# Kernel tuning notes

Hardware: AMD Instinct MI355X
Metric: run time of the kernel (lower is better)

The kernel has to match this reference:

```python
import jax, jax.numpy as jnp
import numpy as np

C = 128         # sphere_channels
H = 512         # hidden_channels
EC = 128        # edge_channels
LMAX = 4
K = 4           # num_experts
N_EQ = 2        # ceil(K/2) equivariant experts
N_NE = 2
N_NODES = 8192
N_EDGES = 262144
DEG_SIZES = np.array([2 * l + 1 for l in range(LMAX + 1)])  # [1,3,5,7,9]
M = int(DEG_SIZES.sum())  # 25 coeffs


def setup_inputs() -> dict:
    key = jax.random.key(0)
    ks = jax.random.split(key, 20)
    s = 0.02
    return {
        "x_emb": jax.random.normal(ks[0], (N_NODES, M, C), jnp.float32),
        "t_ij": jax.random.normal(ks[1], (N_EDGES, EC), jnp.float32),
        "edge_index": jax.random.randint(ks[2], (2, N_EDGES), 0, N_NODES, jnp.int32),
        # equivariant experts (stacked on leading expert axis)
        "eq_w1": jax.random.normal(ks[3], (N_EQ, C, H), jnp.float32) * s,
        "eq_gate_w": jax.random.normal(ks[4], (N_EQ, EC, H * (LMAX + 1)), jnp.float32) * s,
        "eq_gate_b": jax.random.normal(ks[5], (N_EQ, H * (LMAX + 1)), jnp.float32) * s,
        "eq_w2": jax.random.normal(ks[6], (N_EQ, H, C), jnp.float32) * s,
        # non-equivariant experts
        "ne_w1": jax.random.normal(ks[7], (N_NE, C, H), jnp.float32) * s,
        "ne_b1": jax.random.normal(ks[8], (N_NE, H), jnp.float32) * s,
        "ne_gate_w": jax.random.normal(ks[9], (N_NE, EC, H), jnp.float32) * s,
        "ne_gate_b": jax.random.normal(ks[10], (N_NE, H), jnp.float32) * s,
        "ne_w2": jax.random.normal(ks[11], (N_NE, H, C), jnp.float32) * s,
        "ne_b2": jax.random.normal(ks[12], (N_NE, C), jnp.float32) * s,
        # router
        "r_w1": jax.random.normal(ks[13], (EC, EC), jnp.float32) * s,
        "r_b1": jax.random.normal(ks[14], (EC,), jnp.float32) * s,
        "r_w2": jax.random.normal(ks[15], (EC, K), jnp.float32) * s,
        "r_b2": jax.random.normal(ks[16], (K,), jnp.float32) * s,
    }


def reference(x_emb, t_ij, edge_index, eq_w1, eq_gate_w, eq_gate_b, eq_w2,
              ne_w1, ne_b1, ne_gate_w, ne_gate_b, ne_w2, ne_b2,
              r_w1, r_b1, r_w2, r_b2):
    N = x_emb.shape[0]
    silu = jax.nn.silu

    # c_i = scatter-mean of t_ij onto destination nodes
    dst = edge_index[1]
    sums = jax.ops.segment_sum(t_ij, dst, num_segments=N)
    cnt = jax.ops.segment_sum(jnp.ones((t_ij.shape[0],), t_ij.dtype), dst, num_segments=N)
    c = sums / jnp.maximum(cnt, 1.0)[:, None]  # [N, EC]

    # soft routing weights from context
    w = jax.nn.softmax(silu(c @ r_w1 + r_b1) @ r_w2 + r_b2, axis=-1)  # [N, K]

    repeats = jnp.asarray(DEG_SIZES)
    is_scalar = (jnp.arange(M) == 0)[:, None]  # l=0 coeff mask, [M,1]

    # --- equivariant experts (vectorized over expert axis e) ---
    h = jnp.einsum('nmc,ech->enmh', x_emb, eq_w1)                      # [e,N,M,H]
    g = silu(jnp.einsum('nc,ecg->eng', c, eq_gate_w) + eq_gate_b[:, None, :])
    g = g.reshape(N_EQ, N, LMAX + 1, H)
    g = jnp.repeat(g, repeats, axis=2, total_repeat_length=M)          # [e,N,M,H]
    h = jnp.where(is_scalar, silu(h), h) * g                           # SiLU only on l=0
    out_eq = jnp.einsum('enmh,ehc->enmc', h, eq_w2)

    # --- non-equivariant experts ---
    h2 = silu(jnp.einsum('nmc,ech->enmh', x_emb, ne_w1) + ne_b1[:, None, None, :])
    g2 = silu(jnp.einsum('nc,ech->enh', c, ne_gate_w) + ne_gate_b[:, None, :])
    h2 = h2 * g2[:, :, None, :]
    out_ne = jnp.einsum('enmh,ehc->enmc', h2, ne_w2) + ne_b2[:, None, None, :]

    # softmax-weighted mixture (equiv experts first, matching ModuleList order)
    out = (jnp.einsum('nk,knmc->nmc', w[:, :N_EQ], out_eq)
           + jnp.einsum('nk,knmc->nmc', w[:, N_EQ:], out_ne))
    return out
```

## Files before the change

### kernel.cpp

```cpp
#include <hip/hip_runtime.h>

#define NNODES 8192
#define NEDGES 262144
#define CCH    128
#define HCH    512
#define GCOLS  6144
#define ROWS   204800
#define XSPAD  136

typedef __bf16 bf16_t;
typedef __bf16 bf16x8 __attribute__((ext_vector_type(8)));
typedef __bf16 bf16x4 __attribute__((ext_vector_type(4)));
typedef float  f32x4  __attribute__((ext_vector_type(4)));

__device__ __forceinline__ float siluf(float x) {
  return x * __builtin_amdgcn_rcpf(1.f + __expf(-x));
}

#define GLOAD_LDS(g, l) __builtin_amdgcn_global_load_lds( \
    (const __attribute__((address_space(1))) void*)(g), \
    (__attribute__((address_space(3))) void*)(l), 16, 0, 0)

constexpr size_t OFF_CSUM  = 0;
constexpr size_t OFF_DEG   = 4194304;
constexpr size_t OFF_OFFS  = 4227072;
constexpr size_t OFF_CUR   = 4263936;
constexpr size_t OFF_EIDS  = 4296704;
constexpr size_t OFF_WRT   = 5345280;
constexpr size_t OFF_CBF   = 5476352;
constexpr size_t OFF_WPT   = 7573504;
constexpr size_t OFF_BPK   = 9146368;
constexpr size_t OFF_W1T   = 9170944;
constexpr size_t OFF_W2T   = 9695232;
constexpr size_t OFF_GATES = 10219520;

__global__ __launch_bounds__(256) void edge_count_kernel(
    const int* __restrict__ edge_index, int* __restrict__ deg)
{
  int e = blockIdx.x * 256 + threadIdx.x;
  int dst = __builtin_nontemporal_load(&edge_index[NEDGES + e]);
  atomicAdd(&deg[dst], 1);
}

__global__ __launch_bounds__(256) void scan_kernel(
    const int* __restrict__ deg, int* __restrict__ offs, int* __restrict__ cur)
{
  __shared__ int part[256];
  int t = threadIdx.x;
  int s = 0;
  #pragma unroll 4
  for (int i = 0; i < 32; ++i) s += deg[t * 32 + i];
  part[t] = s;
  __syncthreads();
  int incl = s;
  for (int off = 1; off < 256; off <<= 1) {
    int u = (t >= off) ? part[t - off] : 0;
    __syncthreads();
    incl += u;
    part[t] = incl;
    __syncthreads();
  }
  int run = incl - s;
  for (int i = 0; i < 32; ++i) {
    int d = deg[t * 32 + i];
    offs[t * 32 + i] = run;
    cur[t * 32 + i]  = run;
    run += d;
  }
  if (t == 255) offs[8192] = run;
}

__global__ __launch_bounds__(256) void edge_fill_kernel(
    const int* __restrict__ edge_index, int* __restrict__ cur, int* __restrict__ eids)
{
  int e = blockIdx.x * 256 + threadIdx.x;
  int dst = __builtin_nontemporal_load(&edge_index[NEDGES + e]);
  int pos = atomicAdd(&cur[dst], 1);
  eids[pos] = e;
}

__global__ __launch_bounds__(256) void gather_mean_kernel(
    const float* __restrict__ t_ij, const int* __restrict__ offs,
    const int* __restrict__ eids, float* __restrict__ csum, bf16_t* __restrict__ cbf)
{
  __shared__ float red[8][128];
  int n = blockIdx.x, tid = threadIdx.x;
  int sub = tid & 31, rp = tid >> 5;
  int o0 = offs[n], o1 = offs[n + 1];
  f32x4 acc = {0.f, 0.f, 0.f, 0.f};
  for (int j = o0 + rp; j < o1; j += 8) {
    int e = __builtin_nontemporal_load(&eids[j]);
    f32x4 v = __builtin_nontemporal_load((const f32x4*)&t_ij[(size_t)e * CCH + sub * 4]);
    #pragma unroll
    for (int q = 0; q < 4; ++q) acc[q] += v[q];
  }
  *(f32x4*)&red[rp][sub * 4] = acc;
  __syncthreads();
  if (rp == 0) {
    float inv = 1.f / fmaxf((float)(o1 - o0), 1.f);
    f32x4 s = {0.f, 0.f, 0.f, 0.f};
    #pragma unroll
    for (int k = 0; k < 8; ++k) {
      f32x4 r = *(const f32x4*)&red[k][sub * 4];
      #pragma unroll
      for (int q = 0; q < 4; ++q) s[q] += r[q];
    }
    f32x4 m;
    bf16x4 mb;
    #pragma unroll
    for (int q = 0; q < 4; ++q) { m[q] = s[q] * inv; mb[q] = (bf16_t)m[q]; }
    *(f32x4*)&csum[(size_t)n * CCH + sub * 4] = m;
    *(bf16x4*)&cbf[(size_t)n * CCH + sub * 4] = mb;
  }
}

__global__ __launch_bounds__(256) void pack_kernel(
    const float* __restrict__ eq_gate_w, const float* __restrict__ ne_gate_w,
    const float* __restrict__ eq_gate_b, const float* __restrict__ ne_gate_b,
    const float* __restrict__ eq_w1, const float* __restrict__ ne_w1,
    const float* __restrict__ eq_w2, const float* __restrict__ ne_w2,
    bf16_t* __restrict__ WpackT, float* __restrict__ bpack,
    bf16_t* __restrict__ w1T, bf16_t* __restrict__ w2c)
{
  __shared__ float tb[32][33];
  int b = blockIdx.x;
  int tid = threadIdx.x, tx = tid & 31, ty = tid >> 5;
  if (b == 1280) {
    #pragma unroll
    for (int it = 0; it < 24; ++it) {
      int j = it * 256 + tid;
      bpack[j] = (j < 5120) ? eq_gate_b[j] : ne_gate_b[j - 5120];
    }
    return;
  }
  const float* src; bf16_t* dst; int stride; bool w2mode = false;
  int c0, h0; size_t dbase;
  if (b < 640) {
    int e = b / 320, r = b % 320, ct = r / 80, ht = r % 80;
    src = eq_gate_w + (size_t)e * 327680; stride = 2560;
    c0 = ct * 32; h0 = ht * 32;
    dbase = ((size_t)e * 2560 + h0) * 128 + c0; dst = WpackT;
  } else if (b < 768) {
    int bb = b - 640, e = bb / 64, r = bb % 64, ct = r / 16, ht = r % 16;
    src = ne_gate_w + (size_t)e * 65536; stride = 512;
    c0 = ct * 32; h0 = ht * 32;
    dbase = ((size_t)(5120 + e * 512) + h0) * 128 + c0; dst = WpackT;
  } else if (b < 1024) {
    int bb = b - 768, e = bb / 64, r = bb % 64, ct = r / 16, ht = r % 16;
    src = (e < 2) ? eq_w1 + (size_t)e * 65536 : ne_w1 + (size_t)(e - 2) * 65536;
    stride = 512;
    c0 = ct * 32; h0 = ht * 32;
    dbase = ((size_t)(e * 512) + h0) * 128 + c0; dst = w1T;
  } else {
    int bb = b - 1024, e = bb / 64, r = bb % 64, ht = r / 4, ct = r % 4;
    src = (e < 2) ? eq_w2 + (size_t)e * 65536 : ne_w2 + (size_t)(e - 2) * 65536;
    stride = 128; w2mode = true;
    c0 = ct * 32; h0 = ht * 32;
    dbase = (size_t)e * 65536 + (size_t)(ht >> 1) * 8192 + (size_t)c0 * 64 + (size_t)(ht & 1) * 32;
    dst = w2c;
  }
  if (!w2mode) {
    #pragma unroll
    for (int p = 0; p < 4; ++p)
      tb[p * 8 + ty][tx] = src[(size_t)(c0 + p * 8 + ty) * stride + h0 + tx];
    __syncthreads();
    #pragma unroll
    for (int p = 0; p < 4; ++p)
      dst[dbase + (size_t)(p * 8 + ty) * 128 + tx] = (bf16_t)tb[tx][p * 8 + ty];
  } else {
    #pragma unroll
    for (int p = 0; p < 4; ++p)
      tb[p * 8 + ty][tx] = src[(size_t)(h0 + p * 8 + ty) * 128 + c0 + tx];
    __syncthreads();
    #pragma unroll
    for (int p = 0; p < 4; ++p)
      dst[dbase + (size_t)(p * 8 + ty) * 64 + tx] = (bf16_t)tb[tx][p * 8 + ty];
  }
}

__global__ __launch_bounds__(128) void router_kernel(
    const float* __restrict__ c,
    const float* __restrict__ r_w1, const float* __restrict__ r_b1,
    const float* __restrict__ r_w2, const float* __restrict__ r_b2,
    float* __restrict__ wroute)
{
  __shared__ float cl[128];
  __shared__ float h1[128];
  __shared__ float lg[4];
  int n = blockIdx.x, tid = threadIdx.x;
  cl[tid] = c[(size_t)n * 128 + tid];
  __syncthreads();
  float a = 0.f;
  #pragma unroll 8
  for (int k = 0; k < 128; ++k) a += cl[k] * r_w1[k * 128 + tid];
  a += r_b1[tid];
  h1[tid] = siluf(a);
  __syncthreads();
  if (tid < 4) {
    float s = 0.f;
    for (int j = 0; j < 128; ++j) s += h1[j] * r_w2[j * 4 + tid];
    lg[tid] = s + r_b2[tid];
  }
  __syncthreads();
  if (tid == 0) {
    float m = fmaxf(fmaxf(lg[0], lg[1]), fmaxf(lg[2], lg[3]));
    float e0 = __expf(lg[0] - m), e1 = __expf(lg[1] - m);
    float e2 = __expf(lg[2] - m), e3 = __expf(lg[3] - m);
    float s = 1.f / (e0 + e1 + e2 + e3);
    f32x4 w = {e0 * s, e1 * s, e2 * s, e3 * s};
    *(f32x4*)&wroute[n * 4] = w;
  }
}

__global__ __launch_bounds__(256, 2) void gate_gemm_kernel(
    const bf16_t* __restrict__ WpackT, const bf16_t* __restrict__ cbf,
    const float* __restrict__ bpack, const float* __restrict__ wroute,
    bf16_t* __restrict__ gates, int n0)
{
  __shared__ bf16_t gt[128 * XSPAD];
  int jt = blockIdx.x, nt = blockIdx.y;
  int tid = threadIdx.x;
  int wave = tid >> 6, lane = tid & 63;
  int wr = wave >> 1, wc = wave & 1;
  int l15 = lane & 15, quad = lane >> 4;
  int ej = (jt < 20) ? 0 : (jt < 40) ? 1 : (jt < 44) ? 2 : 3;

  f32x4 acc[4][4];
  #pragma unroll
  for (int i = 0; i < 4; ++i)
    #pragma unroll
    for (int j = 0; j < 4; ++j) acc[i][j] = {0.f, 0.f, 0.f, 0.f};

  const bf16_t* abase = WpackT + ((size_t)jt * 128 + wr * 64 + l15) * 128 + quad * 8;
  const bf16_t* bbase = cbf + ((size_t)(n0 + nt * 128) + wc * 64 + l15) * 128 + quad * 8;
  float wsc[4];
  #pragma unroll
  for (int tc = 0; tc < 4; ++tc)
    wsc[tc] = wroute[(size_t)(n0 + nt * 128 + wc * 64 + tc * 16 + l15) * 4 + ej];
  #pragma unroll
  for (int ks = 0; ks < 4; ++ks) {
    bf16x8 af[4], bfr[4];
    #pragma unroll
    for (int tr = 0; tr < 4; ++tr) af[tr] = *(const bf16x8*)(abase + (size_t)tr * 16 * 128 + ks * 32);
    #pragma unroll
    for (int tc = 0; tc < 4; ++tc) bfr[tc] = *(const bf16x8*)(bbase + (size_t)tc * 16 * 128 + ks * 32);
    #pragma unroll
    for (int tr = 0; tr < 4; ++tr)
      #pragma unroll
      for (int tc = 0; tc < 4; ++tc)
        acc[tr][tc] = __builtin_amdgcn_mfma_f32_16x16x32_bf16(af[tr], bfr[tc], acc[tr][tc], 0, 0, 0);
  }
  #pragma unroll
  for (int tr = 0; tr < 4; ++tr) {
    int j0 = wr * 64 + tr * 16 + quad * 4;
    int p0 = wr * 64 + quad * 16 + tr * 4;
    f32x4 bb = *(const f32x4*)&bpack[jt * 128 + j0];
    #pragma unroll
    for (int tc = 0; tc < 4; ++tc) {
      int nl = wc * 64 + tc * 16 + l15;
      f32x4 v = acc[tr][tc];
      bf16x4 gv;
      #pragma unroll
      for (int q = 0; q < 4; ++q) gv[q] = (bf16_t)(siluf(v[q] + bb[q]) * wsc[tc]);
      *(bf16x4*)&gt[nl * XSPAD + p0] = gv;
    }
  }
  __syncthreads();
  #pragma unroll
  for (int it = 0; it < 8; ++it) {
    int idx = it * 2048 + tid * 8;
    int lr = idx >> 7, col = idx & 127;
    *(bf16x8*)&gates[((size_t)nt * 128 + lr) * GCOLS + jt * 128 + col] =
        *(const bf16x8*)&gt[lr * XSPAD + col];
  }
}

__global__ __launch_bounds__(512, 2) void fused_experts_kernel(
    const float* __restrict__ x,
    const bf16_t* __restrict__ w1T,
    const bf16_t* __restrict__ w2c,
    const bf16_t* __restrict__ gates,
    const float* __restrict__ wroute,
    const float* __restrict__ ne_b1,
    const float* __restrict__ ne_b2,
    float* __restrict__ out,
    int n0)
{
  __shared__ __align__(16) bf16_t ws1[8192];
  __shared__ __align__(16) bf16_t ws2[8192];
  __shared__ __align__(16) bf16_t hg[8 * 32 * 64];

  const int tid = threadIdx.x;
  const int wave = tid >> 6, lane = tid & 63;
  const int l15 = lane & 15, quad = lane >> 4;
  const int r0 = n0 * 25 + blockIdx.x * 256;
  const int rbase = wave * 32;
  char* hgw = (char*)(hg + wave * 32 * 64);

  int soff1[2], soff2[2];
  #pragma unroll
  for (int i = 0; i < 2; ++i) {
    int p = wave * 2048 + i * 1024 + lane * 16;
    int row1 = p >> 8;
    soff1[i] = (row1 * 256 + ((p & 255) ^ ((row1 & 7) << 4))) >> 1;
    int row2 = p >> 7;
    soff2[i] = (row2 * 128 + ((p & 127) ^ ((row2 & 7) << 4))) >> 1;
  }
  const int swz = (l15 & 7) << 4;
  int colswz[4];
  #pragma unroll
  for (int ks = 0; ks < 4; ++ks) colswz[ks] = (ks * 64 + quad * 16) ^ swz;

  int nloc[2], lidx[2];
  f32x4 rw[2];
  bf16x8 xf[2][4];
  #pragma unroll
  for (int tc = 0; tc < 2; ++tc) {
    int r = r0 + rbase + tc * 16 + l15;
    int n = r / 25;
    int m = r - n * 25;
    nloc[tc] = n - n0;
    lidx[tc] = (m == 0) ? 0 : (m < 4) ? 1 : (m < 9) ? 2 : (m < 16) ? 3 : 4;
    rw[tc] = *(const f32x4*)&wroute[n * 4];
    const float* xr = x + (size_t)r * CCH + quad * 8;
    #pragma unroll
    for (int ks = 0; ks < 4; ++ks) {
      f32x4 a = __builtin_nontemporal_load((const f32x4*)(xr + ks * 32));
      f32x4 b = __builtin_nontemporal_load((const f32x4*)(xr + ks * 32 + 4));
      bf16x8 v;
      #pragma unroll
      for (int q = 0; q < 4; ++q) { v[q] = (bf16_t)a[q]; v[4 + q] = (bf16_t)b[q]; }
      xf[tc][ks] = v;
    }
  }

  auto gaddr = [&](int tc, int tt) -> const bf16_t* {
    int ee = tt >> 3, hh = tt & 7;
    int base = (ee < 2) ? ee * 2560 + lidx[tc] * 512 : 5120 + (ee - 2) * 512;
    return gates + (nloc[tc] * GCOLS + base + hh * 64 + quad * 16);
  };

  f32x4 oacc[8][2];
  #pragma unroll
  for (int i = 0; i < 8; ++i)
    #pragma unroll
    for (int j = 0; j < 2; ++j) oacc[i][j] = {0.f, 0.f, 0.f, 0.f};

  bf16x8 gnxa[2], gnxb[2];
  #pragma unroll
  for (int tc = 0; tc < 2; ++tc) {
    const bf16_t* gp = gaddr(tc, 0);
    gnxa[tc] = *(const bf16x8*)gp;
    gnxb[tc] = *(const bf16x8*)(gp + 8);
  }
  #pragma unroll
  for (int i = 0; i < 2; ++i) {
    GLOAD_LDS(w1T + soff1[i], ws1 + wave * 1024 + i * 512);
    GLOAD_LDS(w2c + soff2[i], ws2 + wave * 1024 + i * 512);
  }
  __syncthreads();

  #pragma unroll 1
  for (int t = 0; t < 32; ++t) {
    const int e = t >> 3, hc = t & 7;
    const bool is_eq = (e < 2);

    bf16x8 ga[2], gb[2];
    #pragma unroll
    for (int tc = 0; tc < 2; ++tc) { ga[tc] = gnxa[tc]; gb[tc] = gnxb[tc]; }
    if (t < 31) {
      #pragma unroll
      for (int tc = 0; tc < 2; ++tc) {
        const bf16_t* gp = gaddr(tc, t + 1);
        gnxa[tc] = *(const bf16x8*)gp;
        gnxb[tc] = *(const bf16x8*)(gp + 8);
      }
    }

    f32x4 hacc[4][2];
    #pragma unroll
    for (int i = 0; i < 4; ++i)
      #pragma unroll
      for (int j = 0; j < 2; ++j) hacc[i][j] = {0.f, 0.f, 0.f, 0.f};
    #pragma unroll
    for (int ks = 0; ks < 4; ++ks) {
      bf16x8 af[4];
      #pragma unroll
      for (int tr = 0; tr < 4; ++tr)
        af[tr] = *(const bf16x8*)((const char*)ws1 + (l15 + tr * 16) * 256 + colswz[ks]);
      #pragma unroll
      for (int tr = 0; tr < 4; ++tr)
        #pragma unroll
        for (int tc = 0; tc < 2; ++tc)
          hacc[tr][tc] = __builtin_amdgcn_mfma_f32_16x16x32_bf16(af[tr], xf[tc][ks], hacc[tr][tc], 0, 0, 0);
    }
    #pragma unroll
    for (int tc = 0; tc < 2; ++tc) {
      #pragma unroll
      for (int tr = 0; tr < 4; ++tr) {
        int hl = tr * 16 + quad * 4;
        f32x4 v = hacc[tr][tc];
        if (is_eq) {
          if (lidx[tc] == 0) {
            #pragma unroll
            for (int q = 0; q < 4; ++q) v[q] = siluf(v[q]);
          }
        } else {
          f32x4 b1 = *(const f32x4*)&ne_b1[(e - 2) * 512 + hc * 64 + hl];
          #pragma unroll
          for (int q = 0; q < 4; ++q) v[q] = siluf(v[q] + b1[q]);
        }
        bf16x4 hv;
        #pragma unroll
        for (int q = 0; q < 4; ++q) {
          float gf = (float)((tr < 2 ? ga[tc] : gb[tc])[(tr & 1) * 4 + q]);
          hv[q] = (bf16_t)(v[q] * gf);
        }
        *(bf16x4*)(hgw + (tc * 16 + l15) * 128 + ((tr * 32 + quad * 8) ^ swz)) = hv;
      }
    }
    __syncthreads();
    if (t < 31) {
      const bf16_t* g1 = w1T + ((size_t)(t + 1) << 13);
      #pragma unroll
      for (int i = 0; i < 2; ++i)
        GLOAD_LDS(g1 + soff1[i], ws1 + wave * 1024 + i * 512);
    }
    #pragma unroll
    for (int ks = 0; ks < 2; ++ks) {
      bf16x8 bfr[2];
      #pragma unroll
      for (int tc = 0; tc < 2; ++tc)
        bfr[tc] = *(const bf16x8*)(hgw + (tc * 16 + l15) * 128 + ((ks * 64 + quad * 16) ^ swz));
      #pragma unroll
      for (int tr = 0; tr < 8; ++tr) {
        bf16x8 af2 = *(const bf16x8*)((const char*)ws2 + (l15 + tr * 16) * 128 + colswz[ks]);
        #pragma unroll
        for (int tc = 0; tc < 2; ++tc)
          oacc[tr][tc] = __builtin_amdgcn_mfma_f32_16x16x32_bf16(af2, bfr[tc], oacc[tr][tc], 0, 0, 0);
      }
    }
    __syncthreads();
    if (t < 31) {
      const bf16_t* g2 = w2c + ((size_t)(t + 1) << 13);
      #pragma unroll
      for (int i = 0; i < 2; ++i)
        GLOAD_LDS(g2 + soff2[i], ws2 + wave * 1024 + i * 512);
    }
  }
  #pragma unroll
  for (int tc = 0; tc < 2; ++tc) {
    size_t rg = (size_t)(r0 + rbase + tc * 16 + l15);
    float wn0 = rw[tc][2], wn1 = rw[tc][3];
    #pragma unroll
    for (int tr = 0; tr < 8; ++tr) {
      int c0 = tr * 16 + quad * 4;
      f32x4 v = oacc[tr][tc];
      f32x4 b20 = *(const f32x4*)&ne_b2[c0];
      f32x4 b21 = *(const f32x4*)&ne_b2[128 + c0];
      f32x4 ov;
      #pragma unroll
      for (int q = 0; q < 4; ++q)
        ov[q] = v[q] + wn0 * b20[q] + wn1 * b21[q];
      __builtin_nontemporal_store(ov, (f32x4*)&out[rg * CCH + c0]);
    }
  }
}

extern "C" void kernel_launch(void* const* d_in, const int* in_sizes, int n_in,
                              void* d_out, int out_size, void* d_ws, size_t ws_size,
                              hipStream_t stream)
{
  const float* x_emb     = (const float*)d_in[0];
  const float* t_ij      = (const float*)d_in[1];
  const int*   edge_index= (const int*)d_in[2];
  const float* eq_w1     = (const float*)d_in[3];
  const float* eq_gate_w = (const float*)d_in[4];
  const float* eq_gate_b = (const float*)d_in[5];
  const float* eq_w2     = (const float*)d_in[6];
  const float* ne_w1     = (const float*)d_in[7];
  const float* ne_b1     = (const float*)d_in[8];
  const float* ne_gate_w = (const float*)d_in[9];
  const float* ne_gate_b = (const float*)d_in[10];
  const float* ne_w2     = (const float*)d_in[11];
  const float* ne_b2     = (const float*)d_in[12];
  const float* r_w1      = (const float*)d_in[13];
  const float* r_b1      = (const float*)d_in[14];
  const float* r_w2      = (const float*)d_in[15];
  const float* r_b2      = (const float*)d_in[16];
  float* out = (float*)d_out;

  char* ws = (char*)d_ws;
  float*  csum   = (float*)(ws + OFF_CSUM);
  int*    deg    = (int*)(ws + OFF_DEG);
  int*    offs   = (int*)(ws + OFF_OFFS);
  int*    cur    = (int*)(ws + OFF_CUR);
  int*    eids   = (int*)(ws + OFF_EIDS);
  float*  wroute = (float*)(ws + OFF_WRT);
  bf16_t* cbf    = (bf16_t*)(ws + OFF_CBF);
  bf16_t* WpackT = (bf16_t*)(ws + OFF_WPT);
  float*  bpack  = (float*)(ws + OFF_BPK);
  bf16_t* w1T    = (bf16_t*)(ws + OFF_W1T);
  bf16_t* w2c    = (bf16_t*)(ws + OFF_W2T);
  bf16_t* gates  = (bf16_t*)(ws + OFF_GATES);

  size_t avail = (ws_size > OFF_GATES) ? ws_size - OFF_GATES : 0;
  int chunk = 256;
  for (int c = NNODES; c >= 256; c >>= 1) {
    if ((size_t)c * GCOLS * sizeof(bf16_t) <= avail) { chunk = c; break; }
  }

  hipMemsetAsync(ws + OFF_DEG, 0, 32768, stream);

  edge_count_kernel<<<NEDGES / 256, 256, 0, stream>>>(edge_index, deg);
  scan_kernel<<<1, 256, 0, stream>>>(deg, offs, cur);
  edge_fill_kernel<<<NEDGES / 256, 256, 0, stream>>>(edge_index, cur, eids);
  gather_mean_kernel<<<NNODES, 256, 0, stream>>>(t_ij, offs, eids, csum, cbf);

  pack_kernel<<<1281, 256, 0, stream>>>(eq_gate_w, ne_gate_w, eq_gate_b, ne_gate_b,
                                        eq_w1, ne_w1, eq_w2, ne_w2,
                                        WpackT, bpack, w1T, w2c);
  router_kernel<<<NNODES, 128, 0, stream>>>(csum, r_w1, r_b1, r_w2, r_b2, wroute);

  for (int n0 = 0; n0 < NNODES; n0 += chunk) {
    gate_gemm_kernel<<<dim3(GCOLS / 128, chunk / 128), 256, 0, stream>>>(
        WpackT, cbf, bpack, wroute, gates, n0);
    fused_experts_kernel<<<chunk * 25 / 256, 512, 0, stream>>>(
        x_emb, w1T, w2c, gates, wroute, ne_b1, ne_b2, out, n0);
  }
}
```

Baseline: 798.5 us.

## Shrink fused expert blocks to 4 waves and halve hidden-chunk width

The fused experts kernel now runs 256-thread blocks covering 128 rows and processes the hidden dimension in 32-wide chunks (64 iterations instead of 32). The w2 packing layout changes to match, and the software prefetch of the next weight tile is dropped in favour of loading at the start of each iteration followed by a barrier. The intent is smaller LDS use and more blocks per CU for better occupancy, at the cost of twice as many barriers and no overlap between weight loads and MFMA work.

After: 830.7 us. 1.04x slower.

```diff
diff --git a/kernel.cpp b/kernel.cpp
--- a/kernel.cpp
+++ b/kernel.cpp
@@ -156,7 +156,7 @@
     src = (e < 2) ? eq_w2 + (size_t)e * 65536 : ne_w2 + (size_t)(e - 2) * 65536;
     stride = 128; w2mode = true;
     c0 = ct * 32; h0 = ht * 32;
-    dbase = (size_t)e * 65536 + (size_t)(ht >> 1) * 8192 + (size_t)c0 * 64 + (size_t)(ht & 1) * 32;
+    dbase = (size_t)e * 65536 + (size_t)ht * 4096 + (size_t)c0 * 32;
     dst = w2c;
   }
   if (!w2mode) {
@@ -174,7 +174,7 @@
     __syncthreads();
     #pragma unroll
     for (int p = 0; p < 4; ++p)
-      dst[dbase + (size_t)(p * 8 + ty) * 64 + tx] = (bf16_t)tb[tx][p * 8 + ty];
+      dst[dbase + (size_t)(p * 8 + ty) * 32 + tx] = (bf16_t)tb[tx][p * 8 + ty];
   }
 }
 
@@ -275,7 +275,7 @@
   }
 }
 
-__global__ __launch_bounds__(512, 2) void fused_experts_kernel(
+__global__ __launch_bounds__(256, 2) void fused_experts_kernel(
     const float* __restrict__ x,
     const bf16_t* __restrict__ w1T,
     const bf16_t* __restrict__ w2c,
@@ -286,16 +286,16 @@
     float* __restrict__ out,
     int n0)
 {
-  __shared__ __align__(16) bf16_t ws1[8192];
-  __shared__ __align__(16) bf16_t ws2[8192];
-  __shared__ __align__(16) bf16_t hg[8 * 32 * 64];
+  __shared__ __align__(16) bf16_t ws1[4096];
+  __shared__ __align__(16) bf16_t ws2[4096];
+  __shared__ __align__(16) bf16_t hg[4 * 32 * 32];
 
   const int tid = threadIdx.x;
   const int wave = tid >> 6, lane = tid & 63;
   const int l15 = lane & 15, quad = lane >> 4;
-  const int r0 = n0 * 25 + blockIdx.x * 256;
+  const int r0 = n0 * 25 + blockIdx.x * 128;
   const int rbase = wave * 32;
-  char* hgw = (char*)(hg + wave * 32 * 64);
+  char* hgw = (char*)(hg + wave * 32 * 32);
 
   int soff1[2], soff2[2];
   #pragma unroll
@@ -303,13 +303,13 @@
     int p = wave * 2048 + i * 1024 + lane * 16;
     int row1 = p >> 8;
     soff1[i] = (row1 * 256 + ((p & 255) ^ ((row1 & 7) << 4))) >> 1;
-    int row2 = p >> 7;
-    soff2[i] = (row2 * 128 + ((p & 127) ^ ((row2 & 7) << 4))) >> 1;
+    soff2[i] = p >> 1;
   }
   const int swz = (l15 & 7) << 4;
   int colswz[4];
   #pragma unroll
   for (int ks = 0; ks < 4; ++ks) colswz[ks] = (ks * 64 + quad * 16) ^ swz;
+  const int hswz = (l15 & 3) << 4;
 
   int nloc[2], lidx[2];
   f32x4 rw[2];
@@ -335,9 +335,9 @@
   }
 
   auto gaddr = [&](int tc, int tt) -> const bf16_t* {
-    int ee = tt >> 3, hh = tt & 7;
+    int ee = tt >> 4, hh = tt & 15;
     int base = (ee < 2) ? ee * 2560 + lidx[tc] * 512 : 5120 + (ee - 2) * 512;
-    return gates + (nloc[tc] * GCOLS + base + hh * 64 + quad * 16);
+    return gates + (nloc[tc] * GCOLS + base + (hh >> 1) * 64 + (hh & 1) * 8 + quad * 16);
   };
 
   f32x4 oacc[8][2];
@@ -346,50 +346,45 @@
     #pragma unroll
     for (int j = 0; j < 2; ++j) oacc[i][j] = {0.f, 0.f, 0.f, 0.f};
 
-  bf16x8 gnxa[2], gnxb[2];
-  #pragma unroll
-  for (int tc = 0; tc < 2; ++tc) {
-    const bf16_t* gp = gaddr(tc, 0);
-    gnxa[tc] = *(const bf16x8*)gp;
-    gnxb[tc] = *(const bf16x8*)(gp + 8);
-  }
-  #pragma unroll
-  for (int i = 0; i < 2; ++i) {
-    GLOAD_LDS(w1T + soff1[i], ws1 + wave * 1024 + i * 512);
-    GLOAD_LDS(w2c + soff2[i], ws2 + wave * 1024 + i * 512);
-  }
-  __syncthreads();
+  bf16x8 gnx[2];
+  #pragma unroll
+  for (int tc = 0; tc < 2; ++tc) gnx[tc] = *(const bf16x8*)gaddr(tc, 0);
 
   #pragma unroll 1
-  for (int t = 0; t < 32; ++t) {
-    const int e = t >> 3, hc = t & 7;
+  for (int t = 0; t < 64; ++t) {
+    const int e = t >> 4, hh = t & 15;
     const bool is_eq = (e < 2);
 
-    bf16x8 ga[2], gb[2];
-    #pragma unroll
-    for (int tc = 0; tc < 2; ++tc) { ga[tc] = gnxa[tc]; gb[tc] = gnxb[tc]; }
-    if (t < 31) {
-      #pragma unroll
-      for (int tc = 0; tc < 2; ++tc) {
-        const bf16_t* gp = gaddr(tc, t + 1);
-        gnxa[tc] = *(const bf16x8*)gp;
-        gnxb[tc] = *(const bf16x8*)(gp + 8);
-      }
-    }
-
-    f32x4 hacc[4][2];
-    #pragma unroll
-    for (int i = 0; i < 4; ++i)
+    const bf16_t* g1 = w1T + ((size_t)t << 12);
+    const bf16_t* g2 = w2c + ((size_t)t << 12);
+    #pragma unroll
+    for (int i = 0; i < 2; ++i) {
+      GLOAD_LDS(g1 + soff1[i], ws1 + wave * 1024 + i * 512);
+      GLOAD_LDS(g2 + soff2[i], ws2 + wave * 1024 + i * 512);
+    }
+    __syncthreads();
+
+    bf16x8 ga[2];
+    #pragma unroll
+    for (int tc = 0; tc < 2; ++tc) ga[tc] = gnx[tc];
+    if (t < 63) {
+      #pragma unroll
+      for (int tc = 0; tc < 2; ++tc) gnx[tc] = *(const bf16x8*)gaddr(tc, t + 1);
+    }
+
+    f32x4 hacc[2][2];
+    #pragma unroll
+    for (int i = 0; i < 2; ++i)
       #pragma unroll
       for (int j = 0; j < 2; ++j) hacc[i][j] = {0.f, 0.f, 0.f, 0.f};
     #pragma unroll
     for (int ks = 0; ks < 4; ++ks) {
-      bf16x8 af[4];
-      #pragma unroll
-      for (int tr = 0; tr < 4; ++tr)
+      bf16x8 af[2];
+      #pragma unroll
+      for (int tr = 0; tr < 2; ++tr)
         af[tr] = *(const bf16x8*)((const char*)ws1 + (l15 + tr * 16) * 256 + colswz[ks]);
       #pragma unroll
-      for (int tr = 0; tr < 4; ++tr)
+      for (int tr = 0; tr < 2; ++tr)
         #pragma unroll
         for (int tc = 0; tc < 2; ++tc)
           hacc[tr][tc] = __builtin_amdgcn_mfma_f32_16x16x32_bf16(af[tr], xf[tc][ks], hacc[tr][tc], 0, 0, 0);
@@ -397,7 +392,7 @@
     #pragma unroll
     for (int tc = 0; tc < 2; ++tc) {
       #pragma unroll
-      for (int tr = 0; tr < 4; ++tr) {
+      for (int tr = 0; tr < 2; ++tr) {
         int hl = tr * 16 + quad * 4;
         f32x4 v = hacc[tr][tc];
         if (is_eq) {
@@ -406,47 +401,32 @@
             for (int q = 0; q < 4; ++q) v[q] = siluf(v[q]);
           }
         } else {
-          f32x4 b1 = *(const f32x4*)&ne_b1[(e - 2) * 512 + hc * 64 + hl];
+          f32x4 b1 = *(const f32x4*)&ne_b1[(e - 2) * 512 + hh * 32 + hl];
           #pragma unroll
           for (int q = 0; q < 4; ++q) v[q] = siluf(v[q] + b1[q]);
         }
         bf16x4 hv;
         #pragma unroll
         for (int q = 0; q < 4; ++q) {
-          float gf = (float)((tr < 2 ? ga[tc] : gb[tc])[(tr & 1) * 4 + q]);
+          float gf = (float)ga[tc][tr * 4 + q];
           hv[q] = (bf16_t)(v[q] * gf);
         }
-        *(bf16x4*)(hgw + (tc * 16 + l15) * 128 + ((tr * 32 + quad * 8) ^ swz)) = hv;
+        *(bf16x4*)(hgw + (tc * 16 + l15) * 64 + ((tr * 32 + quad * 8) ^ hswz)) = hv;
       }
     }
+    __builtin_amdgcn_wave_barrier();
+    bf16x8 bfr[2];
+    #pragma unroll
+    for (int tc = 0; tc < 2; ++tc)
+      bfr[tc] = *(const bf16x8*)(hgw + (tc * 16 + l15) * 64 + ((quad * 16) ^ hswz));
+    #pragma unroll
+    for (int tr = 0; tr < 8; ++tr) {
+      bf16x8 af2 = *(const bf16x8*)((const char*)ws2 + (l15 + tr * 16) * 64 + quad * 16);
+      #pragma unroll
+      for (int tc = 0; tc < 2; ++tc)
+        oacc[tr][tc] = __builtin_amdgcn_mfma_f32_16x16x32_bf16(af2, bfr[tc], oacc[tr][tc], 0, 0, 0);
+    }
     __syncthreads();
-    if (t < 31) {
-      const bf16_t* g1 = w1T + ((size_t)(t + 1) << 13);
-      #pragma unroll
-      for (int i = 0; i < 2; ++i)
-        GLOAD_LDS(g1 + soff1[i], ws1 + wave * 1024 + i * 512);
-    }
-    #pragma unroll
-    for (int ks = 0; ks < 2; ++ks) {
-      bf16x8 bfr[2];
-      #pragma unroll
-      for (int tc = 0; tc < 2; ++tc)
-        bfr[tc] = *(const bf16x8*)(hgw + (tc * 16 + l15) * 128 + ((ks * 64 + quad * 16) ^ swz));
-      #pragma unroll
-      for (int tr = 0; tr < 8; ++tr) {
-        bf16x8 af2 = *(const bf16x8*)((const char*)ws2 + (l15 + tr * 16) * 128 + colswz[ks]);
-        #pragma unroll
-        for (int tc = 0; tc < 2; ++tc)
-          oacc[tr][tc] = __builtin_amdgcn_mfma_f32_16x16x32_bf16(af2, bfr[tc], oacc[tr][tc], 0, 0, 0);
-      }
-    }
-    __syncthreads();
-    if (t < 31) {
-      const bf16_t* g2 = w2c + ((size_t)(t + 1) << 13);
-      #pragma unroll
-      for (int i = 0; i < 2; ++i)
-        GLOAD_LDS(g2 + soff2[i], ws2 + wave * 1024 + i * 512);
-    }
   }
   #pragma unroll
   for (int tc = 0; tc < 2; ++tc) {
@@ -505,8 +485,8 @@
   bf16_t* gates  = (bf16_t*)(ws + OFF_GATES);
 
   size_t avail = (ws_size > OFF_GATES) ? ws_size - OFF_GATES : 0;
-  int chunk = 256;
-  for (int c = NNODES; c >= 256; c >>= 1) {
+  int chunk = 128;
+  for (int c = NNODES; c >= 128; c >>= 1) {
     if ((size_t)c * GCOLS * sizeof(bf16_t) <= avail) { chunk = c; break; }
   }
 
@@ -525,7 +505,7 @@
   for (int n0 = 0; n0 < NNODES; n0 += chunk) {
     gate_gemm_kernel<<<dim3(GCOLS / 128, chunk / 128), 256, 0, stream>>>(
         WpackT, cbf, bpack, wroute, gates, n0);
-    fused_experts_kernel<<<chunk * 25 / 256, 512, 0, stream>>>(
+    fused_experts_kernel<<<chunk * 25 / 128, 256, 0, stream>>>(
         x_emb, w1T, w2c, gates, wroute, ne_b1, ne_b2, out, n0);
   }
 }
```
